# Optimization experiments

Hardware: AMD Instinct MI355X
Metric: run time of the kernel (lower is better)

The kernel has to match this reference:

```python
import jax, jax.numpy as jnp
import numpy as np

N_NODES = 100000
N_EDGES = 1600000
IN_DIM = 128
OUT_DIM = 128
LEAKY_SLOPE = 0.01  # torch nn.LeakyReLU default


def setup_inputs() -> dict:
    key = jax.random.key(0)
    k1, k2, k3, k4 = jax.random.split(key, 4)
    x = jax.random.normal(k1, (N_NODES, IN_DIM), dtype=jnp.float32)
    edge_index = jax.random.randint(k2, (2, N_EDGES), 0, N_NODES, dtype=jnp.int64)
    edge_attr = jax.random.uniform(k3, (N_EDGES,), dtype=jnp.float32)
    # Linear params (xavier_uniform weight, zero bias)
    limit = np.sqrt(6.0 / (IN_DIM + OUT_DIM)).astype(np.float32)
    W = jax.random.uniform(k4, (OUT_DIM, IN_DIM), minval=-limit, maxval=limit, dtype=jnp.float32)
    b = jnp.zeros((OUT_DIM,), dtype=jnp.float32)
    return {"x": x, "edge_index": edge_index, "edge_attr": edge_attr, "W": W, "b": b}


def reference(x, edge_index, edge_attr, W, b):
    src = edge_index[0]  # x_j (source nodes)
    dst = edge_index[1]  # aggregation index (target nodes)
    # message: gather source features, scale by per-edge scalar  [E, D]
    msg = x[src] * edge_attr[:, None]
    # aggregate: scatter-add over target index  [N, D]
    agg = jax.ops.segment_sum(msg, dst, num_segments=N_NODES)
    # update: Linear + LeakyReLU (dropout is identity at p=0 / eval)
    out = agg @ W.T + b
    return jnp.where(out >= 0, out, LEAKY_SLOPE * out)
```

## Files before the change

### kernel.cpp

```cpp
#include <hip/hip_runtime.h>

#define N_NODES 100000
#define N_EDGES 1600000
#define DIM 128
#define LEAKY 0.01f
#define RS_STRIDE 132
#define WS_STRIDE 132
#define NBUCKET 391
#define SB_EDGES 4096
#define NSB 391

typedef short bf16x8 __attribute__((ext_vector_type(8)));
typedef float f32x4 __attribute__((ext_vector_type(4)));

static __device__ __forceinline__ unsigned short f2bf(float f) {
  unsigned int u = __float_as_uint(f);
  u = (u + 0x7fffu + ((u >> 16) & 1u)) >> 16;
  return (unsigned short)u;
}

__global__ __launch_bounds__(512) void sort_local_kernel(
    const int* __restrict__ ei, const float* __restrict__ attr,
    int2* __restrict__ binned, unsigned short* __restrict__ counts,
    int* __restrict__ srcOff) {
  __shared__ int hist[NBUCKET];
  __shared__ int cursor[NBUCKET];
  __shared__ int scanBuf[512];
  __shared__ int2 stage[SB_EDGES];

  const int t = threadIdx.x;
  const int blk = blockIdx.x;
  const int base = blk * SB_EDGES;
  const int n = min(SB_EDGES, N_EDGES - base);

  if (t < NBUCKET) hist[t] = 0;
  __syncthreads();

  int myP[8];
  int myB[8];
  float myA[8];
#pragma unroll
  for (int k = 0; k < 8; ++k) {
    int i = t + k * 512;
    if (i < n) {
      int e = base + i;
      int s = ei[e];
      int d = ei[N_EDGES + e];
      myA[k] = attr[e];
      myB[k] = d >> 8;
      myP[k] = s | ((d & 255) << 17);
      atomicAdd(&hist[myB[k]], 1);
    } else {
      myB[k] = -1;
    }
  }
  __syncthreads();

  int v = (t < NBUCKET) ? hist[t] : 0;
  scanBuf[t] = v;
  __syncthreads();
  for (int off = 1; off < 512; off <<= 1) {
    int u = (t >= off) ? scanBuf[t - off] : 0;
    __syncthreads();
    scanBuf[t] += u;
    __syncthreads();
  }
  if (t < NBUCKET) {
    int excl = scanBuf[t] - v;
    cursor[t] = excl;
    counts[(size_t)t * NSB + blk] = (unsigned short)v;
    srcOff[(size_t)t * NSB + blk] = base + excl;
  }
  __syncthreads();

#pragma unroll
  for (int k = 0; k < 8; ++k) {
    if (myB[k] >= 0) {
      int loc = atomicAdd(&cursor[myB[k]], 1);
      stage[loc] = make_int2(myP[k], __float_as_int(myA[k]));
    }
  }
  __syncthreads();

  for (int i = t; i < n; i += 512) binned[base + i] = stage[i];
}

__global__ __launch_bounds__(128) void bucket_count_kernel(
    const unsigned short* __restrict__ counts, int* __restrict__ bucketCount,
    const float* __restrict__ W, bf16x8* __restrict__ wfrag,
    const float4* __restrict__ x4, ushort4* __restrict__ xb4) {
  __shared__ int red[128];
  const int b = blockIdx.x;
  const int t = threadIdx.x;

  if (b < NBUCKET) {
    int s = 0;
    for (int sb = t; sb < NSB; sb += 128) s += counts[(size_t)b * NSB + sb];
    red[t] = s;
    __syncthreads();
    for (int off = 64; off > 0; off >>= 1) {
      if (t < off) red[t] += red[t + off];
      __syncthreads();
    }
    if (t == 0) bucketCount[b] = red[0];
  } else {
    const int gid = (b - NBUCKET) * 128 + t;
    const int lane = gid & 63;
    const int q = (gid >> 6) & 3;
    const int nt = gid >> 8;
    const int n = nt * 16 + (lane & 15);
    const int kb = q * 32 + ((lane >> 4) & 3) * 8;
    const float4 f0 = *(const float4*)(W + n * DIM + kb);
    const float4 f1 = *(const float4*)(W + n * DIM + kb + 4);
    bf16x8 frag;
    frag[0] = (short)f2bf(f0.x); frag[1] = (short)f2bf(f0.y);
    frag[2] = (short)f2bf(f0.z); frag[3] = (short)f2bf(f0.w);
    frag[4] = (short)f2bf(f1.x); frag[5] = (short)f2bf(f1.y);
    frag[6] = (short)f2bf(f1.z); frag[7] = (short)f2bf(f1.w);
    wfrag[gid] = frag;
  }

  if (xb4) {
    const int stride = (NBUCKET + 16) * 128;
    for (int i = b * 128 + t; i < (N_NODES * DIM) / 4; i += stride) {
      float4 vv = x4[i];
      ushort4 o;
      o.x = f2bf(vv.x); o.y = f2bf(vv.y); o.z = f2bf(vv.z); o.w = f2bf(vv.w);
      xb4[i] = o;
    }
  }
}

__global__ __launch_bounds__(512) void bucket_scan_kernel(
    const int* __restrict__ bucketCount, int* __restrict__ bucketBase) {
  __shared__ int s[512];
  const int t = threadIdx.x;
  int v = (t < NBUCKET) ? bucketCount[t] : 0;
  s[t] = v;
  __syncthreads();
  for (int off = 1; off < 512; off <<= 1) {
    int u = (t >= off) ? s[t - off] : 0;
    __syncthreads();
    s[t] += u;
    __syncthreads();
  }
  if (t < NBUCKET) bucketBase[t] = s[t] - v;
}

__global__ __launch_bounds__(448) void passB_kernel(
    const int2* __restrict__ binned, const unsigned short* __restrict__ counts,
    const int* __restrict__ srcOff, const int* __restrict__ bucketBase,
    int2* __restrict__ csr, int* __restrict__ row_ptr) {
  __shared__ int runSrc[NSB];
  __shared__ int runLen[NSB];
  __shared__ int hist[256];
  __shared__ int cur[256];
  __shared__ int scanBuf[256];

  const int b = blockIdx.x;
  const int t = threadIdx.x;

  if (t < NSB) {
    runSrc[t] = srcOff[(size_t)b * NSB + t];
    runLen[t] = (int)counts[(size_t)b * NSB + t];
  }
  if (t < 256) hist[t] = 0;
  __syncthreads();

  if (t < NSB) {
    const int src = runSrc[t];
    const int len = runLen[t];
    for (int j = 0; j < len; ++j) {
      int px = binned[src + j].x;
      atomicAdd(&hist[(px >> 17) & 255], 1);
    }
  }
  __syncthreads();

  int hv = (t < 256) ? hist[t] : 0;
  if (t < 256) scanBuf[t] = hv;
  __syncthreads();
  for (int off = 1; off < 256; off <<= 1) {
    int u = 0;
    if (t < 256 && t >= off) u = scanBuf[t - off];
    __syncthreads();
    if (t < 256) scanBuf[t] += u;
    __syncthreads();
  }
  const int bb = bucketBase[b];
  if (t < 256) {
    int excl = scanBuf[t] - hv;
    cur[t] = excl;
    int node = b * 256 + t;
    if (node < N_NODES) row_ptr[node] = bb + excl;
  }
  if (b == 0 && t == 0) row_ptr[N_NODES] = N_EDGES;
  __syncthreads();

  if (t < NSB) {
    const int src = runSrc[t];
    const int len = runLen[t];
    for (int j = 0; j < len; ++j) {
      int2 rec = binned[src + j];
      int ld = (rec.x >> 17) & 255;
      int pos = bb + atomicAdd(&cur[ld], 1);
      csr[pos] = make_int2(rec.x & 0x1FFFF, rec.y);
    }
  }
}

__global__ __launch_bounds__(256) void gather_aggb_kernel(
    const unsigned short* __restrict__ xb, const int* __restrict__ row_ptr,
    const int2* __restrict__ csr, unsigned int* __restrict__ aggB) {
  const int w = threadIdx.x >> 6;
  const int lane = threadIdx.x & 63;
  const int nA = blockIdx.x * 8 + w * 2;
  const int nB = nA + 1;

  int a = row_ptr[nA];
  const int aEnd = row_ptr[nA + 1];
  int b = row_ptr[nB];
  const int bEnd = row_ptr[nB + 1];

  float2 accA = make_float2(0.f, 0.f);
  float2 accB = make_float2(0.f, 0.f);

  while (a + 5 < aEnd && b + 5 < bEnd) {
    int2 ea[6], eb[6];
#pragma unroll
    for (int k = 0; k < 6; ++k) {
      ea[k] = csr[a + k];
      eb[k] = csr[b + k];
    }
    unsigned int ua[6], ub[6];
#pragma unroll
    for (int k = 0; k < 6; ++k) {
      ua[k] = *(const unsigned int*)(xb + (size_t)ea[k].x * DIM + lane * 2);
      ub[k] = *(const unsigned int*)(xb + (size_t)eb[k].x * DIM + lane * 2);
    }
#pragma unroll
    for (int k = 0; k < 6; ++k) {
      float fa = __int_as_float(ea[k].y);
      float fb = __int_as_float(eb[k].y);
      accA.x += __uint_as_float(ua[k] << 16) * fa;
      accA.y += __uint_as_float(ua[k] & 0xffff0000u) * fa;
      accB.x += __uint_as_float(ub[k] << 16) * fb;
      accB.y += __uint_as_float(ub[k] & 0xffff0000u) * fb;
    }
    a += 6;
    b += 6;
  }

  for (; a + 3 < aEnd; a += 4) {
    int2 e[4];
#pragma unroll
    for (int k = 0; k < 4; ++k) e[k] = csr[a + k];
    unsigned int u[4];
#pragma unroll
    for (int k = 0; k < 4; ++k)
      u[k] = *(const unsigned int*)(xb + (size_t)e[k].x * DIM + lane * 2);
#pragma unroll
    for (int k = 0; k < 4; ++k) {
      float f = __int_as_float(e[k].y);
      accA.x += __uint_as_float(u[k] << 16) * f;
      accA.y += __uint_as_float(u[k] & 0xffff0000u) * f;
    }
  }
  for (; a < aEnd; ++a) {
    int2 e0 = csr[a];
    float f0 = __int_as_float(e0.y);
    unsigned int u0 = *(const unsigned int*)(xb + (size_t)e0.x * DIM + lane * 2);
    accA.x += __uint_as_float(u0 << 16) * f0;
    accA.y += __uint_as_float(u0 & 0xffff0000u) * f0;
  }

  for (; b + 3 < bEnd; b += 4) {
    int2 e[4];
#pragma unroll
    for (int k = 0; k < 4; ++k) e[k] = csr[b + k];
    unsigned int u[4];
#pragma unroll
    for (int k = 0; k < 4; ++k)
      u[k] = *(const unsigned int*)(xb + (size_t)e[k].x * DIM + lane * 2);
#pragma unroll
    for (int k = 0; k < 4; ++k) {
      float f = __int_as_float(e[k].y);
      accB.x += __uint_as_float(u[k] << 16) * f;
      accB.y += __uint_as_float(u[k] & 0xffff0000u) * f;
    }
  }
  for (; b < bEnd; ++b) {
    int2 e0 = csr[b];
    float f0 = __int_as_float(e0.y);
    unsigned int u0 = *(const unsigned int*)(xb + (size_t)e0.x * DIM + lane * 2);
    accB.x += __uint_as_float(u0 << 16) * f0;
    accB.y += __uint_as_float(u0 & 0xffff0000u) * f0;
  }

  aggB[(size_t)nA * 64 + lane] =
      (unsigned int)f2bf(accA.x) | ((unsigned int)f2bf(accA.y) << 16);
  aggB[(size_t)nB * 64 + lane] =
      (unsigned int)f2bf(accB.x) | ((unsigned int)f2bf(accB.y) << 16);
}

__global__ __launch_bounds__(256) void gather_bf16_kernel(
    const unsigned short* __restrict__ xb, const int* __restrict__ row_ptr,
    const int2* __restrict__ csr, float* __restrict__ out) {
  const int node = blockIdx.x * 4 + (threadIdx.x >> 6);
  const int lane = threadIdx.x & 63;

  const int beg = row_ptr[node];
  const int end = row_ptr[node + 1];

  float2 acc = make_float2(0.f, 0.f);
  int e = beg;
  for (; e + 3 < end; e += 4) {
    int2 e0 = csr[e];
    int2 e1 = csr[e + 1];
    int2 e2 = csr[e + 2];
    int2 e3 = csr[e + 3];
    unsigned int u0 = *(const unsigned int*)(xb + (size_t)e0.x * DIM + lane * 2);
    unsigned int u1 = *(const unsigned int*)(xb + (size_t)e1.x * DIM + lane * 2);
    unsigned int u2 = *(const unsigned int*)(xb + (size_t)e2.x * DIM + lane * 2);
    unsigned int u3 = *(const unsigned int*)(xb + (size_t)e3.x * DIM + lane * 2);
    float a0 = __int_as_float(e0.y), a1 = __int_as_float(e1.y);
    float a2 = __int_as_float(e2.y), a3 = __int_as_float(e3.y);
    acc.x += __uint_as_float(u0 << 16) * a0;
    acc.y += __uint_as_float(u0 & 0xffff0000u) * a0;
    acc.x += __uint_as_float(u1 << 16) * a1;
    acc.y += __uint_as_float(u1 & 0xffff0000u) * a1;
    acc.x += __uint_as_float(u2 << 16) * a2;
    acc.y += __uint_as_float(u2 & 0xffff0000u) * a2;
    acc.x += __uint_as_float(u3 << 16) * a3;
    acc.y += __uint_as_float(u3 & 0xffff0000u) * a3;
  }
  for (; e < end; ++e) {
    int2 e0 = csr[e];
    float a0 = __int_as_float(e0.y);
    unsigned int u0 = *(const unsigned int*)(xb + (size_t)e0.x * DIM + lane * 2);
    acc.x += __uint_as_float(u0 << 16) * a0;
    acc.y += __uint_as_float(u0 & 0xffff0000u) * a0;
  }
  *(float2*)(out + (size_t)node * DIM + lane * 2) = acc;
}

__global__ __launch_bounds__(256) void gather_f32_kernel(
    const float* __restrict__ x, const int* __restrict__ row_ptr,
    const int2* __restrict__ csr, float* __restrict__ out) {
  const int node = blockIdx.x * 4 + (threadIdx.x >> 6);
  const int lane = threadIdx.x & 63;

  const int beg = row_ptr[node];
  const int end = row_ptr[node + 1];

  float2 acc = make_float2(0.f, 0.f);
  int e = beg;
  for (; e + 3 < end; e += 4) {
    int2 e0 = csr[e];
    int2 e1 = csr[e + 1];
    int2 e2 = csr[e + 2];
    int2 e3 = csr[e + 3];
    float2 v0 = *(const float2*)(x + (size_t)e0.x * DIM + lane * 2);
    float2 v1 = *(const float2*)(x + (size_t)e1.x * DIM + lane * 2);
    float2 v2 = *(const float2*)(x + (size_t)e2.x * DIM + lane * 2);
    float2 v3 = *(const float2*)(x + (size_t)e3.x * DIM + lane * 2);
    float a0 = __int_as_float(e0.y), a1 = __int_as_float(e1.y);
    float a2 = __int_as_float(e2.y), a3 = __int_as_float(e3.y);
    acc.x += v0.x * a0; acc.y += v0.y * a0;
    acc.x += v1.x * a1; acc.y += v1.y * a1;
    acc.x += v2.x * a2; acc.y += v2.y * a2;
    acc.x += v3.x * a3; acc.y += v3.y * a3;
  }
  for (; e < end; ++e) {
    int2 e0 = csr[e];
    float a0 = __int_as_float(e0.y);
    float2 v0 = *(const float2*)(x + (size_t)e0.x * DIM + lane * 2);
    acc.x += v0.x * a0; acc.y += v0.y * a0;
  }
  *(float2*)(out + (size_t)node * DIM + lane * 2) = acc;
}

__global__ __launch_bounds__(256) void linear_mfma_bf16_kernel(
    const unsigned short* __restrict__ aggB, const bf16x8* __restrict__ wfrag,
    const float* __restrict__ bias, float* __restrict__ out) {
  const int wave = threadIdx.x >> 6;
  const int lane = threadIdx.x & 63;
  const int r0 = (blockIdx.x * 4 + wave) * 16;
  if (r0 >= N_NODES) return;

  const int m = lane & 15;
  const int quad = lane >> 4;
  const int row = r0 + m;

  bf16x8 afrag[4];
#pragma unroll
  for (int q = 0; q < 4; ++q) {
    afrag[q] = *(const bf16x8*)(aggB + (size_t)row * DIM + q * 32 + quad * 8);
  }

#pragma unroll
  for (int nt = 0; nt < 8; ++nt) {
    const float bv = bias[nt * 16 + m];
    f32x4 acc = {bv, bv, bv, bv};
#pragma unroll
    for (int q = 0; q < 4; ++q) {
      bf16x8 bfrag = wfrag[(nt * 4 + q) * 64 + lane];
      acc = __builtin_amdgcn_mfma_f32_16x16x32_bf16(afrag[q], bfrag, acc, 0, 0, 0);
    }
    const int col = nt * 16 + m;
#pragma unroll
    for (int i = 0; i < 4; ++i) {
      float v = acc[i];
      v = v >= 0.f ? v : v * LEAKY;
      out[(size_t)(r0 + quad * 4 + i) * DIM + col] = v;
    }
  }
}

__global__ __launch_bounds__(256) void linear_mfma_kernel(
    const float* __restrict__ agg, const bf16x8* __restrict__ wfrag,
    const float* __restrict__ bias, float* __restrict__ out) {
  const int wave = threadIdx.x >> 6;
  const int lane = threadIdx.x & 63;
  const int r0 = (blockIdx.x * 4 + wave) * 16;
  if (r0 >= N_NODES) return;

  const int m = lane & 15;
  const int quad = lane >> 4;
  const int row = r0 + m;

  bf16x8 afrag[4];
#pragma unroll
  for (int q = 0; q < 4; ++q) {
    const float* ap = agg + (size_t)row * DIM + q * 32 + quad * 8;
    const float4 f0 = *(const float4*)(ap);
    const float4 f1 = *(const float4*)(ap + 4);
    afrag[q][0] = (short)f2bf(f0.x); afrag[q][1] = (short)f2bf(f0.y);
    afrag[q][2] = (short)f2bf(f0.z); afrag[q][3] = (short)f2bf(f0.w);
    afrag[q][4] = (short)f2bf(f1.x); afrag[q][5] = (short)f2bf(f1.y);
    afrag[q][6] = (short)f2bf(f1.z); afrag[q][7] = (short)f2bf(f1.w);
  }

#pragma unroll
  for (int nt = 0; nt < 8; ++nt) {
    const float bv = bias[nt * 16 + m];
    f32x4 acc = {bv, bv, bv, bv};
#pragma unroll
    for (int q = 0; q < 4; ++q) {
      bf16x8 bfrag = wfrag[(nt * 4 + q) * 64 + lane];
      acc = __builtin_amdgcn_mfma_f32_16x16x32_bf16(afrag[q], bfrag, acc, 0, 0, 0);
    }
    const int col = nt * 16 + m;
#pragma unroll
    for (int i = 0; i < 4; ++i) {
      float v = acc[i];
      v = v >= 0.f ? v : v * LEAKY;
      out[(size_t)(r0 + quad * 4 + i) * DIM + col] = v;
    }
  }
}

__global__ __launch_bounds__(256) void scatter_kernel(
    const float* __restrict__ x, const int* __restrict__ ei,
    const float* __restrict__ attr, float* __restrict__ agg) {
  int gid = blockIdx.x * blockDim.x + threadIdx.x;
  int e = gid >> 5;
  int f = (gid & 31) * 4;
  if (e >= N_EDGES) return;
  int s = ei[e];
  int d = ei[N_EDGES + e];
  float a = attr[e];
  const float4 xv = *(const float4*)(x + (size_t)s * DIM + f);
  float* dp = agg + (size_t)d * DIM + f;
  atomicAdd(dp + 0, xv.x * a);
  atomicAdd(dp + 1, xv.y * a);
  atomicAdd(dp + 2, xv.z * a);
  atomicAdd(dp + 3, xv.w * a);
}

__global__ __launch_bounds__(256, 2) void linear_kernel(
    const float* __restrict__ agg, const float* __restrict__ W,
    const float* __restrict__ bias, float* __restrict__ out) {
  __shared__ float Rs[32 * RS_STRIDE];
  __shared__ float Ws[64 * WS_STRIDE];

  const int tid = threadIdx.x;
  const int c = (tid & 31) * 4;
  const int rg = tid >> 5;
  const size_t rowBase = (size_t)blockIdx.x * 32;

  {
    const int lr = tid >> 3;
    const int col = (tid & 7) * 16;
    const float4* src = (const float4*)(agg + (rowBase + lr) * DIM + col);
#pragma unroll
    for (int j = 0; j < 4; ++j) {
      *(float4*)(Rs + lr * RS_STRIDE + col + j * 4) = src[j];
    }
  }

  const float4 bv = *(const float4*)(bias + c);
  float4 acc0 = bv, acc1 = bv, acc2 = bv, acc3 = bv;

  for (int half = 0; half < 2; ++half) {
    __syncthreads();
    {
      const int k0 = tid >> 7;
      const int o = tid & 127;
#pragma unroll
      for (int kk = k0; kk < 64; kk += 2) {
        Ws[kk * WS_STRIDE + o] = W[o * DIM + half * 64 + kk];
      }
    }
    __syncthreads();

    const float* rs0 = Rs + (rg * 4 + 0) * RS_STRIDE + half * 64;
    const float* rs1 = Rs + (rg * 4 + 1) * RS_STRIDE + half * 64;
    const float* rs2 = Rs + (rg * 4 + 2) * RS_STRIDE + half * 64;
    const float* rs3 = Rs + (rg * 4 + 3) * RS_STRIDE + half * 64;

#pragma unroll 8
    for (int k4 = 0; k4 < 16; ++k4) {
      const float4 v0 = *(const float4*)(rs0 + k4 * 4);
      const float4 v1 = *(const float4*)(rs1 + k4 * 4);
      const float4 v2 = *(const float4*)(rs2 + k4 * 4);
      const float4 v3 = *(const float4*)(rs3 + k4 * 4);
      const float4 w0 = *(const float4*)(Ws + (k4 * 4 + 0) * WS_STRIDE + c);
      const float4 w1 = *(const float4*)(Ws + (k4 * 4 + 1) * WS_STRIDE + c);
      const float4 w2 = *(const float4*)(Ws + (k4 * 4 + 2) * WS_STRIDE + c);
      const float4 w3 = *(const float4*)(Ws + (k4 * 4 + 3) * WS_STRIDE + c);

#define FMA4(acc, v)                                               \
      acc.x += v.x * w0.x + v.y * w1.x + v.z * w2.x + v.w * w3.x;  \
      acc.y += v.x * w0.y + v.y * w1.y + v.z * w2.y + v.w * w3.y;  \
      acc.z += v.x * w0.z + v.y * w1.z + v.z * w2.z + v.w * w3.z;  \
      acc.w += v.x * w0.w + v.y * w1.w + v.z * w2.w + v.w * w3.w;
      FMA4(acc0, v0)
      FMA4(acc1, v1)
      FMA4(acc2, v2)
      FMA4(acc3, v3)
#undef FMA4
    }
  }

#define LEAKY4(acc)                                   \
  acc.x = acc.x >= 0.f ? acc.x : acc.x * LEAKY;       \
  acc.y = acc.y >= 0.f ? acc.y : acc.y * LEAKY;       \
  acc.z = acc.z >= 0.f ? acc.z : acc.z * LEAKY;       \
  acc.w = acc.w >= 0.f ? acc.w : acc.w * LEAKY;
  LEAKY4(acc0) LEAKY4(acc1) LEAKY4(acc2) LEAKY4(acc3)
#undef LEAKY4

  const int row0 = (int)rowBase + rg * 4;
  *(float4*)(out + (size_t)(row0 + 0) * DIM + c) = acc0;
  *(float4*)(out + (size_t)(row0 + 1) * DIM + c) = acc1;
  *(float4*)(out + (size_t)(row0 + 2) * DIM + c) = acc2;
  *(float4*)(out + (size_t)(row0 + 3) * DIM + c) = acc3;
}

extern "C" void kernel_launch(void* const* d_in, const int* in_sizes, int n_in,
                              void* d_out, int out_size, void* d_ws, size_t ws_size,
                              hipStream_t stream) {
  const float* x = (const float*)d_in[0];
  const int* ei = (const int*)d_in[1];
  const float* attr = (const float*)d_in[2];
  const float* W = (const float*)d_in[3];
  const float* b = (const float*)d_in[4];
  float* out = (float*)d_out;

  const size_t offBinned = 0;
  const size_t offCounts = 12812288;
  const size_t offSrcOff = offCounts + 305920;
  const size_t offBCount = offSrcOff + 611584;
  const size_t offBBase  = offBCount + 1792;
  const size_t offCsr    = offBBase + 1792;
  const size_t offRowPtr = offCsr + 12812288;
  const size_t offWfrag  = offRowPtr + 400128;
  const size_t sortNeed  = offWfrag + 32768;
  const size_t offXb     = sortNeed;
  const size_t fullNeed  = offXb + 25600000;
  const size_t offAggB   = fullNeed;
  const size_t bf16Need  = offAggB + 25600000;

  if (ws_size >= sortNeed) {
    char* ws = (char*)d_ws;
    int2* binned = (int2*)(ws + offBinned);
    unsigned short* counts = (unsigned short*)(ws + offCounts);
    int* srcOff = (int*)(ws + offSrcOff);
    int* bucketCount = (int*)(ws + offBCount);
    int* bucketBase = (int*)(ws + offBBase);
    int2* csr = (int2*)(ws + offCsr);
    int* row_ptr = (int*)(ws + offRowPtr);
    bf16x8* wfrag = (bf16x8*)(ws + offWfrag);
    const bool haveXb = ws_size >= fullNeed;
    const bool haveAggB = ws_size >= bf16Need;
    unsigned short* xb = haveXb ? (unsigned short*)(ws + offXb) : nullptr;
    unsigned int* aggB = haveAggB ? (unsigned int*)(ws + offAggB) : nullptr;

    sort_local_kernel<<<NSB, 512, 0, stream>>>(ei, attr, binned, counts, srcOff);
    bucket_count_kernel<<<NBUCKET + 16, 128, 0, stream>>>(
        counts, bucketCount, W, wfrag, (const float4*)x, (ushort4*)xb);
    bucket_scan_kernel<<<1, 512, 0, stream>>>(bucketCount, bucketBase);
    passB_kernel<<<NBUCKET, 448, 0, stream>>>(binned, counts, srcOff, bucketBase,
                                              csr, row_ptr);
    if (haveAggB) {
      gather_aggb_kernel<<<N_NODES / 8, 256, 0, stream>>>(xb, row_ptr, csr, aggB);
      linear_mfma_bf16_kernel<<<(N_NODES + 63) / 64, 256, 0, stream>>>(
          (const unsigned short*)aggB, wfrag, b, out);
    } else if (haveXb) {
      gather_bf16_kernel<<<N_NODES / 4, 256, 0, stream>>>(xb, row_ptr, csr, out);
      linear_mfma_kernel<<<(N_NODES + 63) / 64, 256, 0, stream>>>(out, wfrag, b, out);
    } else {
      gather_f32_kernel<<<N_NODES / 4, 256, 0, stream>>>(x, row_ptr, csr, out);
      linear_mfma_kernel<<<(N_NODES + 63) / 64, 256, 0, stream>>>(out, wfrag, b, out);
    }
  } else {
    hipMemsetAsync(out, 0, (size_t)N_NODES * DIM * sizeof(float), stream);
    scatter_kernel<<<(N_EDGES * 32) / 256, 256, 0, stream>>>(x, ei, attr, out);
    linear_kernel<<<N_NODES / 32, 256, 0, stream>>>(out, W, b, out);
  }
}
```

Before: 246.8 us.

## Replace two-pass bucket sort CSR build with global atomic counting sort

Replaces the local-sort-plus-bucket-merge CSR construction with a direct counting sort. It builds a global degree histogram with atomics, scans it into row pointers, and places each edge through an atomicAdd on a per-node cursor. The x-to-bf16 and W-fragment conversions become separate kernels, and the fallback gather/linear variants are removed. This drops the intermediate binned array and the serial per-run loops in passB. In exchange it relies on heavy global atomics and scattered writes, and edge order within a row becomes nondeterministic.

```diff
diff --git a/kernel.cpp b/kernel.cpp
--- a/kernel.cpp
+++ b/kernel.cpp
@@ -7,8 +7,6 @@
 #define RS_STRIDE 132
 #define WS_STRIDE 132
 #define NBUCKET 391
-#define SB_EDGES 4096
-#define NSB 391
 
 typedef short bf16x8 __attribute__((ext_vector_type(8)));
 typedef float f32x4 __attribute__((ext_vector_type(4)));
@@ -19,116 +17,31 @@
   return (unsigned short)u;
 }
 
-__global__ __launch_bounds__(512) void sort_local_kernel(
-    const int* __restrict__ ei, const float* __restrict__ attr,
-    int2* __restrict__ binned, unsigned short* __restrict__ counts,
-    int* __restrict__ srcOff) {
-  __shared__ int hist[NBUCKET];
-  __shared__ int cursor[NBUCKET];
-  __shared__ int scanBuf[512];
-  __shared__ int2 stage[SB_EDGES];
-
-  const int t = threadIdx.x;
-  const int blk = blockIdx.x;
-  const int base = blk * SB_EDGES;
-  const int n = min(SB_EDGES, N_EDGES - base);
-
-  if (t < NBUCKET) hist[t] = 0;
-  __syncthreads();
-
-  int myP[8];
-  int myB[8];
-  float myA[8];
-#pragma unroll
-  for (int k = 0; k < 8; ++k) {
-    int i = t + k * 512;
-    if (i < n) {
-      int e = base + i;
-      int s = ei[e];
-      int d = ei[N_EDGES + e];
-      myA[k] = attr[e];
-      myB[k] = d >> 8;
-      myP[k] = s | ((d & 255) << 17);
-      atomicAdd(&hist[myB[k]], 1);
-    } else {
-      myB[k] = -1;
-    }
-  }
-  __syncthreads();
-
-  int v = (t < NBUCKET) ? hist[t] : 0;
-  scanBuf[t] = v;
-  __syncthreads();
-  for (int off = 1; off < 512; off <<= 1) {
-    int u = (t >= off) ? scanBuf[t - off] : 0;
-    __syncthreads();
-    scanBuf[t] += u;
-    __syncthreads();
-  }
-  if (t < NBUCKET) {
-    int excl = scanBuf[t] - v;
-    cursor[t] = excl;
-    counts[(size_t)t * NSB + blk] = (unsigned short)v;
-    srcOff[(size_t)t * NSB + blk] = base + excl;
-  }
-  __syncthreads();
-
-#pragma unroll
-  for (int k = 0; k < 8; ++k) {
-    if (myB[k] >= 0) {
-      int loc = atomicAdd(&cursor[myB[k]], 1);
-      stage[loc] = make_int2(myP[k], __float_as_int(myA[k]));
-    }
-  }
-  __syncthreads();
-
-  for (int i = t; i < n; i += 512) binned[base + i] = stage[i];
-}
-
-__global__ __launch_bounds__(128) void bucket_count_kernel(
-    const unsigned short* __restrict__ counts, int* __restrict__ bucketCount,
-    const float* __restrict__ W, bf16x8* __restrict__ wfrag,
-    const float4* __restrict__ x4, ushort4* __restrict__ xb4) {
-  __shared__ int red[128];
+__global__ __launch_bounds__(256) void deg_hist_kernel(
+    const int* __restrict__ ei, int* __restrict__ deg) {
+  const int e = blockIdx.x * 256 + threadIdx.x;
+  const int d = ei[N_EDGES + e];
+  atomicAdd(&deg[d], 1);
+}
+
+__global__ __launch_bounds__(256) void scanA_kernel(
+    const int* __restrict__ deg, int* __restrict__ row_ptr,
+    int* __restrict__ bucketCount) {
+  __shared__ int s[256];
   const int b = blockIdx.x;
   const int t = threadIdx.x;
-
-  if (b < NBUCKET) {
-    int s = 0;
-    for (int sb = t; sb < NSB; sb += 128) s += counts[(size_t)b * NSB + sb];
-    red[t] = s;
-    __syncthreads();
-    for (int off = 64; off > 0; off >>= 1) {
-      if (t < off) red[t] += red[t + off];
-      __syncthreads();
-    }
-    if (t == 0) bucketCount[b] = red[0];
-  } else {
-    const int gid = (b - NBUCKET) * 128 + t;
-    const int lane = gid & 63;
-    const int q = (gid >> 6) & 3;
-    const int nt = gid >> 8;
-    const int n = nt * 16 + (lane & 15);
-    const int kb = q * 32 + ((lane >> 4) & 3) * 8;
-    const float4 f0 = *(const float4*)(W + n * DIM + kb);
-    const float4 f1 = *(const float4*)(W + n * DIM + kb + 4);
-    bf16x8 frag;
-    frag[0] = (short)f2bf(f0.x); frag[1] = (short)f2bf(f0.y);
-    frag[2] = (short)f2bf(f0.z); frag[3] = (short)f2bf(f0.w);
-    frag[4] = (short)f2bf(f1.x); frag[5] = (short)f2bf(f1.y);
-    frag[6] = (short)f2bf(f1.z); frag[7] = (short)f2bf(f1.w);
-    wfrag[gid] = frag;
-  }
-
-  if (xb4) {
-    const int stride = (NBUCKET + 16) * 128;
-    for (int i = b * 128 + t; i < (N_NODES * DIM) / 4; i += stride) {
-      float4 vv = x4[i];
-      ushort4 o;
-      o.x = f2bf(vv.x); o.y = f2bf(vv.y); o.z = f2bf(vv.z); o.w = f2bf(vv.w);
-      xb4[i] = o;
-    }
-  }
+  const int node = b * 256 + t;
+  const int v = (node < N_NODES) ? deg[node] : 0;
+  s[t] = v;
+  __syncthreads();
+  for (int off = 1; off < 256; off <<= 1) {
+    int u = (t >= off) ? s[t - off] : 0;
+    __syncthreads();
+    s[t] += u;
+    __syncthreads();
+  }
+  if (node < N_NODES) row_ptr[node] = s[t] - v;
+  if (t == 0) bucketCount[b] = s[255];
 }
 
 __global__ __launch_bounds__(512) void bucket_scan_kernel(
@@ -147,66 +60,56 @@
   if (t < NBUCKET) bucketBase[t] = s[t] - v;
 }
 
-__global__ __launch_bounds__(448) void passB_kernel(
-    const int2* __restrict__ binned, const unsigned short* __restrict__ counts,
-    const int* __restrict__ srcOff, const int* __restrict__ bucketBase,
-    int2* __restrict__ csr, int* __restrict__ row_ptr) {
-  __shared__ int runSrc[NSB];
-  __shared__ int runLen[NSB];
-  __shared__ int hist[256];
-  __shared__ int cur[256];
-  __shared__ int scanBuf[256];
-
+__global__ __launch_bounds__(256) void scanB_kernel(
+    int* __restrict__ row_ptr, const int* __restrict__ bucketBase,
+    int* __restrict__ cur) {
   const int b = blockIdx.x;
   const int t = threadIdx.x;
-
-  if (t < NSB) {
-    runSrc[t] = srcOff[(size_t)b * NSB + t];
-    runLen[t] = (int)counts[(size_t)b * NSB + t];
-  }
-  if (t < 256) hist[t] = 0;
-  __syncthreads();
-
-  if (t < NSB) {
-    const int src = runSrc[t];
-    const int len = runLen[t];
-    for (int j = 0; j < len; ++j) {
-      int px = binned[src + j].x;
-      atomicAdd(&hist[(px >> 17) & 255], 1);
-    }
-  }
-  __syncthreads();
-
-  int hv = (t < 256) ? hist[t] : 0;
-  if (t < 256) scanBuf[t] = hv;
-  __syncthreads();
-  for (int off = 1; off < 256; off <<= 1) {
-    int u = 0;
-    if (t < 256 && t >= off) u = scanBuf[t - off];
-    __syncthreads();
-    if (t < 256) scanBuf[t] += u;
-    __syncthreads();
-  }
-  const int bb = bucketBase[b];
-  if (t < 256) {
-    int excl = scanBuf[t] - hv;
-    cur[t] = excl;
-    int node = b * 256 + t;
-    if (node < N_NODES) row_ptr[node] = bb + excl;
+  const int node = b * 256 + t;
+  if (node < N_NODES) {
+    const int rp = row_ptr[node] + bucketBase[b];
+    row_ptr[node] = rp;
+    cur[node] = rp;
   }
   if (b == 0 && t == 0) row_ptr[N_NODES] = N_EDGES;
-  __syncthreads();
-
-  if (t < NSB) {
-    const int src = runSrc[t];
-    const int len = runLen[t];
-    for (int j = 0; j < len; ++j) {
-      int2 rec = binned[src + j];
-      int ld = (rec.x >> 17) & 255;
-      int pos = bb + atomicAdd(&cur[ld], 1);
-      csr[pos] = make_int2(rec.x & 0x1FFFF, rec.y);
-    }
-  }
+}
+
+__global__ __launch_bounds__(256) void place_edges_kernel(
+    const int* __restrict__ ei, const float* __restrict__ attr,
+    int* __restrict__ cur, int2* __restrict__ csr) {
+  const int e = blockIdx.x * 256 + threadIdx.x;
+  const int s = ei[e];
+  const int d = ei[N_EDGES + e];
+  const float a = attr[e];
+  const int pos = atomicAdd(&cur[d], 1);
+  csr[pos] = make_int2(s, __float_as_int(a));
+}
+
+__global__ __launch_bounds__(256) void x2b_kernel(
+    const float4* __restrict__ x, ushort4* __restrict__ xb) {
+  const int i = blockIdx.x * 256 + threadIdx.x;
+  float4 v = x[i];
+  ushort4 o;
+  o.x = f2bf(v.x); o.y = f2bf(v.y); o.z = f2bf(v.z); o.w = f2bf(v.w);
+  xb[i] = o;
+}
+
+__global__ __launch_bounds__(256) void w_frag_kernel(
+    const float* __restrict__ W, bf16x8* __restrict__ wfrag) {
+  const int gid = blockIdx.x * 256 + threadIdx.x;
+  const int lane = gid & 63;
+  const int q = (gid >> 6) & 3;
+  const int nt = gid >> 8;
+  const int n = nt * 16 + (lane & 15);
+  const int kb = q * 32 + ((lane >> 4) & 3) * 8;
+  const float4 f0 = *(const float4*)(W + n * DIM + kb);
+  const float4 f1 = *(const float4*)(W + n * DIM + kb + 4);
+  bf16x8 frag;
+  frag[0] = (short)f2bf(f0.x); frag[1] = (short)f2bf(f0.y);
+  frag[2] = (short)f2bf(f0.z); frag[3] = (short)f2bf(f0.w);
+  frag[4] = (short)f2bf(f1.x); frag[5] = (short)f2bf(f1.y);
+  frag[6] = (short)f2bf(f1.z); frag[7] = (short)f2bf(f1.w);
+  wfrag[gid] = frag;
 }
 
 __global__ __launch_bounds__(256) void gather_aggb_kernel(
@@ -303,83 +206,6 @@
       (unsigned int)f2bf(accB.x) | ((unsigned int)f2bf(accB.y) << 16);
 }
 
-__global__ __launch_bounds__(256) void gather_bf16_kernel(
-    const unsigned short* __restrict__ xb, const int* __restrict__ row_ptr,
-    const int2* __restrict__ csr, float* __restrict__ out) {
-  const int node = blockIdx.x * 4 + (threadIdx.x >> 6);
-  const int lane = threadIdx.x & 63;
-
-  const int beg = row_ptr[node];
-  const int end = row_ptr[node + 1];
-
-  float2 acc = make_float2(0.f, 0.f);
-  int e = beg;
-  for (; e + 3 < end; e += 4) {
-    int2 e0 = csr[e];
-    int2 e1 = csr[e + 1];
-    int2 e2 = csr[e + 2];
-    int2 e3 = csr[e + 3];
-    unsigned int u0 = *(const unsigned int*)(xb + (size_t)e0.x * DIM + lane * 2);
-    unsigned int u1 = *(const unsigned int*)(xb + (size_t)e1.x * DIM + lane * 2);
-    unsigned int u2 = *(const unsigned int*)(xb + (size_t)e2.x * DIM + lane * 2);
-    unsigned int u3 = *(const unsigned int*)(xb + (size_t)e3.x * DIM + lane * 2);
-    float a0 = __int_as_float(e0.y), a1 = __int_as_float(e1.y);
-    float a2 = __int_as_float(e2.y), a3 = __int_as_float(e3.y);
-    acc.x += __uint_as_float(u0 << 16) * a0;
-    acc.y += __uint_as_float(u0 & 0xffff0000u) * a0;
-    acc.x += __uint_as_float(u1 << 16) * a1;
-    acc.y += __uint_as_float(u1 & 0xffff0000u) * a1;
-    acc.x += __uint_as_float(u2 << 16) * a2;
-    acc.y += __uint_as_float(u2 & 0xffff0000u) * a2;
-    acc.x += __uint_as_float(u3 << 16) * a3;
-    acc.y += __uint_as_float(u3 & 0xffff0000u) * a3;
-  }
-  for (; e < end; ++e) {
-    int2 e0 = csr[e];
-    float a0 = __int_as_float(e0.y);
-    unsigned int u0 = *(const unsigned int*)(xb + (size_t)e0.x * DIM + lane * 2);
-    acc.x += __uint_as_float(u0 << 16) * a0;
-    acc.y += __uint_as_float(u0 & 0xffff0000u) * a0;
-  }
-  *(float2*)(out + (size_t)node * DIM + lane * 2) = acc;
-}
-
-__global__ __launch_bounds__(256) void gather_f32_kernel(
-    const float* __restrict__ x, const int* __restrict__ row_ptr,
-    const int2* __restrict__ csr, float* __restrict__ out) {
-  const int node = blockIdx.x * 4 + (threadIdx.x >> 6);
-  const int lane = threadIdx.x & 63;
-
-  const int beg = row_ptr[node];
-  const int end = row_ptr[node + 1];
-
-  float2 acc = make_float2(0.f, 0.f);
-  int e = beg;
-  for (; e + 3 < end; e += 4) {
-    int2 e0 = csr[e];
-    int2 e1 = csr[e + 1];
-    int2 e2 = csr[e + 2];
-    int2 e3 = csr[e + 3];
-    float2 v0 = *(const float2*)(x + (size_t)e0.x * DIM + lane * 2);
-    float2 v1 = *(const float2*)(x + (size_t)e1.x * DIM + lane * 2);
-    float2 v2 = *(const float2*)(x + (size_t)e2.x * DIM + lane * 2);
-    float2 v3 = *(const float2*)(x + (size_t)e3.x * DIM + lane * 2);
-    float a0 = __int_as_float(e0.y), a1 = __int_as_float(e1.y);
-    float a2 = __int_as_float(e2.y), a3 = __int_as_float(e3.y);
-    acc.x += v0.x * a0; acc.y += v0.y * a0;
-    acc.x += v1.x * a1; acc.y += v1.y * a1;
-    acc.x += v2.x * a2; acc.y += v2.y * a2;
-    acc.x += v3.x * a3; acc.y += v3.y * a3;
-  }
-  for (; e < end; ++e) {
-    int2 e0 = csr[e];
-    float a0 = __int_as_float(e0.y);
-    float2 v0 = *(const float2*)(x + (size_t)e0.x * DIM + lane * 2);
-    acc.x += v0.x * a0; acc.y += v0.y * a0;
-  }
-  *(float2*)(out + (size_t)node * DIM + lane * 2) = acc;
-}
-
 __global__ __launch_bounds__(256) void linear_mfma_bf16_kernel(
     const unsigned short* __restrict__ aggB, const bf16x8* __restrict__ wfrag,
     const float* __restrict__ bias, float* __restrict__ out) {
@@ -396,49 +222,6 @@
 #pragma unroll
   for (int q = 0; q < 4; ++q) {
     afrag[q] = *(const bf16x8*)(aggB + (size_t)row * DIM + q * 32 + quad * 8);
-  }
-
-#pragma unroll
-  for (int nt = 0; nt < 8; ++nt) {
-    const float bv = bias[nt * 16 + m];
-    f32x4 acc = {bv, bv, bv, bv};
-#pragma unroll
-    for (int q = 0; q < 4; ++q) {
-      bf16x8 bfrag = wfrag[(nt * 4 + q) * 64 + lane];
-      acc = __builtin_amdgcn_mfma_f32_16x16x32_bf16(afrag[q], bfrag, acc, 0, 0, 0);
-    }
-    const int col = nt * 16 + m;
-#pragma unroll
-    for (int i = 0; i < 4; ++i) {
-      float v = acc[i];
-      v = v >= 0.f ? v : v * LEAKY;
-      out[(size_t)(r0 + quad * 4 + i) * DIM + col] = v;
-    }
-  }
-}
-
-__global__ __launch_bounds__(256) void linear_mfma_kernel(
-    const float* __restrict__ agg, const bf16x8* __restrict__ wfrag,
-    const float* __restrict__ bias, float* __restrict__ out) {
-  const int wave = threadIdx.x >> 6;
-  const int lane = threadIdx.x & 63;
-  const int r0 = (blockIdx.x * 4 + wave) * 16;
-  if (r0 >= N_NODES) return;
-
-  const int m = lane & 15;
-  const int quad = lane >> 4;
-  const int row = r0 + m;
-
-  bf16x8 afrag[4];
-#pragma unroll
-  for (int q = 0; q < 4; ++q) {
-    const float* ap = agg + (size_t)row * DIM + q * 32 + quad * 8;
-    const float4 f0 = *(const float4*)(ap);
-    const float4 f1 = *(const float4*)(ap + 4);
-    afrag[q][0] = (short)f2bf(f0.x); afrag[q][1] = (short)f2bf(f0.y);
-    afrag[q][2] = (short)f2bf(f0.z); afrag[q][3] = (short)f2bf(f0.w);
-    afrag[q][4] = (short)f2bf(f1.x); afrag[q][5] = (short)f2bf(f1.y);
-    afrag[q][6] = (short)f2bf(f1.z); afrag[q][7] = (short)f2bf(f1.w);
   }
 
 #pragma unroll
@@ -568,52 +351,40 @@
   const float* b = (const float*)d_in[4];
   float* out = (float*)d_out;
 
-  const size_t offBinned = 0;
-  const size_t offCounts = 12812288;
-  const size_t offSrcOff = offCounts + 305920;
-  const size_t offBCount = offSrcOff + 611584;
+  const size_t offCsr    = 0;
+  const size_t offRowPtr = 12800000;
+  const size_t offDeg    = offRowPtr + 400128;
+  const size_t offCur    = offDeg + 400128;
+  const size_t offBCount = offCur + 400128;
   const size_t offBBase  = offBCount + 1792;
-  const size_t offCsr    = offBBase + 1792;
-  const size_t offRowPtr = offCsr + 12812288;
-  const size_t offWfrag  = offRowPtr + 400128;
-  const size_t sortNeed  = offWfrag + 32768;
-  const size_t offXb     = sortNeed;
-  const size_t fullNeed  = offXb + 25600000;
-  const size_t offAggB   = fullNeed;
-  const size_t bf16Need  = offAggB + 25600000;
-
-  if (ws_size >= sortNeed) {
+  const size_t offWfrag  = offBBase + 1792;
+  const size_t offXb     = offWfrag + 32768;
+  const size_t offAggB   = offXb + 25600000;
+  const size_t fullNeed  = offAggB + 25600000;
+
+  if (ws_size >= fullNeed) {
     char* ws = (char*)d_ws;
-    int2* binned = (int2*)(ws + offBinned);
-    unsigned short* counts = (unsigned short*)(ws + offCounts);
-    int* srcOff = (int*)(ws + offSrcOff);
+    int2* csr = (int2*)(ws + offCsr);
+    int* row_ptr = (int*)(ws + offRowPtr);
+    int* deg = (int*)(ws + offDeg);
+    int* cur = (int*)(ws + offCur);
     int* bucketCount = (int*)(ws + offBCount);
     int* bucketBase = (int*)(ws + offBBase);
-    int2* csr = (int2*)(ws + offCsr);
-    int* row_ptr = (int*)(ws + offRowPtr);
     bf16x8* wfrag = (bf16x8*)(ws + offWfrag);
-    const bool haveXb = ws_size >= fullNeed;
-    const bool haveAggB = ws_size >= bf16Need;
-    unsigned short* xb = haveXb ? (unsigned short*)(ws + offXb) : nullptr;
-    unsigned int* aggB = haveAggB ? (unsigned int*)(ws + offAggB) : nullptr;
-
-    sort_local_kernel<<<NSB, 512, 0, stream>>>(ei, attr, binned, counts, srcOff);
-    bucket_count_kernel<<<NBUCKET + 16, 128, 0, stream>>>(
-        counts, bucketCount, W, wfrag, (const float4*)x, (ushort4*)xb);
+    unsigned short* xb = (unsigned short*)(ws + offXb);
+    unsigned int* aggB = (unsigned int*)(ws + offAggB);
+
+    hipMemsetAsync(deg, 0, (size_t)N_NODES * sizeof(int), stream);
+    deg_hist_kernel<<<N_EDGES / 256, 256, 0, stream>>>(ei, deg);
+    scanA_kernel<<<NBUCKET, 256, 0, stream>>>(deg, row_ptr, bucketCount);
     bucket_scan_kernel<<<1, 512, 0, stream>>>(bucketCount, bucketBase);
-    passB_kernel<<<NBUCKET, 448, 0, stream>>>(binned, counts, srcOff, bucketBase,
-                                              csr, row_ptr);
-    if (haveAggB) {
-      gather_aggb_kernel<<<N_NODES / 8, 256, 0, stream>>>(xb, row_ptr, csr, aggB);
-      linear_mfma_bf16_kernel<<<(N_NODES + 63) / 64, 256, 0, stream>>>(
-          (const unsigned short*)aggB, wfrag, b, out);
-    } else if (haveXb) {
-      gather_bf16_kernel<<<N_NODES / 4, 256, 0, stream>>>(xb, row_ptr, csr, out);
-      linear_mfma_kernel<<<(N_NODES + 63) / 64, 256, 0, stream>>>(out, wfrag, b, out);
-    } else {
-      gather_f32_kernel<<<N_NODES / 4, 256, 0, stream>>>(x, row_ptr, csr, out);
-      linear_mfma_kernel<<<(N_NODES + 63) / 64, 256, 0, stream>>>(out, wfrag, b, out);
-    }
+    scanB_kernel<<<NBUCKET, 256, 0, stream>>>(row_ptr, bucketBase, cur);
+    place_edges_kernel<<<N_EDGES / 256, 256, 0, stream>>>(ei, attr, cur, csr);
+    x2b_kernel<<<12500, 256, 0, stream>>>((const float4*)x, (ushort4*)xb);
+    w_frag_kernel<<<8, 256, 0, stream>>>(W, wfrag);
+    gather_aggb_kernel<<<N_NODES / 8, 256, 0, stream>>>(xb, row_ptr, csr, aggB);
+    linear_mfma_bf16_kernel<<<(N_NODES + 63) / 64, 256, 0, stream>>>(
+        (const unsigned short*)aggB, wfrag, b, out);
   } else {
     hipMemsetAsync(out, 0, (size_t)N_NODES * DIM * sizeof(float), stream);
     scatter_kernel<<<(N_EDGES * 32) / 256, 256, 0, stream>>>(x, ei, attr, out);
```

Result: slower. 379.2 us (+53.7%).

## Fuse bucket count, scan, and CSR build into one kernel with conversions

Applied to the files above, without the earlier changes.

Removes the separate bucket_count and bucket_scan kernels. Each CSR-build block now computes its own bucket base by summing all preceding counts directly. The W-fragment and x-to-bf16 conversions run as extra blocks in the same launch, which cuts two kernel launches and their serialization gaps. In exchange, each bucket block does a redundant prefix sum over up to ~150K counts, with total work growing quadratically across blocks, and the conversion blocks compete with the build blocks for the GPU.

```diff
diff --git a/kernel.cpp b/kernel.cpp
--- a/kernel.cpp
+++ b/kernel.cpp
@@ -9,6 +9,7 @@
 #define NBUCKET 391
 #define SB_EDGES 4096
 #define NSB 391
+#define X2B_CHUNKS 7143
 
 typedef short bf16x8 __attribute__((ext_vector_type(8)));
 typedef float f32x4 __attribute__((ext_vector_type(4)));
@@ -85,87 +86,76 @@
   for (int i = t; i < n; i += 512) binned[base + i] = stage[i];
 }
 
-__global__ __launch_bounds__(128) void bucket_count_kernel(
-    const unsigned short* __restrict__ counts, int* __restrict__ bucketCount,
-    const float* __restrict__ W, bf16x8* __restrict__ wfrag,
-    const float4* __restrict__ x4, ushort4* __restrict__ xb4) {
-  __shared__ int red[128];
-  const int b = blockIdx.x;
+__global__ __launch_bounds__(448) void build_convert_kernel(
+    const int2* __restrict__ binned, const unsigned short* __restrict__ counts,
+    const int* __restrict__ srcOff, int2* __restrict__ csr,
+    int* __restrict__ row_ptr, const float* __restrict__ W,
+    bf16x8* __restrict__ wfrag, const float4* __restrict__ x4,
+    ushort4* __restrict__ xb4) {
+  const int blk = blockIdx.x;
   const int t = threadIdx.x;
 
-  if (b < NBUCKET) {
-    int s = 0;
-    for (int sb = t; sb < NSB; sb += 128) s += counts[(size_t)b * NSB + sb];
-    red[t] = s;
-    __syncthreads();
-    for (int off = 64; off > 0; off >>= 1) {
-      if (t < off) red[t] += red[t + off];
-      __syncthreads();
-    }
-    if (t == 0) bucketCount[b] = red[0];
-  } else {
-    const int gid = (b - NBUCKET) * 128 + t;
-    const int lane = gid & 63;
-    const int q = (gid >> 6) & 3;
-    const int nt = gid >> 8;
-    const int n = nt * 16 + (lane & 15);
-    const int kb = q * 32 + ((lane >> 4) & 3) * 8;
-    const float4 f0 = *(const float4*)(W + n * DIM + kb);
-    const float4 f1 = *(const float4*)(W + n * DIM + kb + 4);
-    bf16x8 frag;
-    frag[0] = (short)f2bf(f0.x); frag[1] = (short)f2bf(f0.y);
-    frag[2] = (short)f2bf(f0.z); frag[3] = (short)f2bf(f0.w);
-    frag[4] = (short)f2bf(f1.x); frag[5] = (short)f2bf(f1.y);
-    frag[6] = (short)f2bf(f1.z); frag[7] = (short)f2bf(f1.w);
-    wfrag[gid] = frag;
-  }
-
-  if (xb4) {
-    const int stride = (NBUCKET + 16) * 128;
-    for (int i = b * 128 + t; i < (N_NODES * DIM) / 4; i += stride) {
-      float4 vv = x4[i];
-      ushort4 o;
-      o.x = f2bf(vv.x); o.y = f2bf(vv.y); o.z = f2bf(vv.z); o.w = f2bf(vv.w);
-      xb4[i] = o;
-    }
-  }
-}
-
-__global__ __launch_bounds__(512) void bucket_scan_kernel(
-    const int* __restrict__ bucketCount, int* __restrict__ bucketBase) {
-  __shared__ int s[512];
-  const int t = threadIdx.x;
-  int v = (t < NBUCKET) ? bucketCount[t] : 0;
-  s[t] = v;
-  __syncthreads();
-  for (int off = 1; off < 512; off <<= 1) {
-    int u = (t >= off) ? s[t - off] : 0;
-    __syncthreads();
-    s[t] += u;
-    __syncthreads();
-  }
-  if (t < NBUCKET) bucketBase[t] = s[t] - v;
-}
-
-__global__ __launch_bounds__(448) void passB_kernel(
-    const int2* __restrict__ binned, const unsigned short* __restrict__ counts,
-    const int* __restrict__ srcOff, const int* __restrict__ bucketBase,
-    int2* __restrict__ csr, int* __restrict__ row_ptr) {
+  if (blk >= NBUCKET) {
+    if (blk < NBUCKET + 8) {
+      if (t < 256) {
+        const int gid = (blk - NBUCKET) * 256 + t;
+        const int lane = gid & 63;
+        const int q = (gid >> 6) & 3;
+        const int nt = gid >> 8;
+        const int n = nt * 16 + (lane & 15);
+        const int kb = q * 32 + ((lane >> 4) & 3) * 8;
+        const float4 f0 = *(const float4*)(W + n * DIM + kb);
+        const float4 f1 = *(const float4*)(W + n * DIM + kb + 4);
+        bf16x8 frag;
+        frag[0] = (short)f2bf(f0.x); frag[1] = (short)f2bf(f0.y);
+        frag[2] = (short)f2bf(f0.z); frag[3] = (short)f2bf(f0.w);
+        frag[4] = (short)f2bf(f1.x); frag[5] = (short)f2bf(f1.y);
+        frag[6] = (short)f2bf(f1.z); frag[7] = (short)f2bf(f1.w);
+        wfrag[gid] = frag;
+      }
+    } else {
+      const int i = (blk - NBUCKET - 8) * 448 + t;
+      if (i < (N_NODES * DIM) / 4) {
+        float4 vv = x4[i];
+        ushort4 o;
+        o.x = f2bf(vv.x); o.y = f2bf(vv.y); o.z = f2bf(vv.z); o.w = f2bf(vv.w);
+        xb4[i] = o;
+      }
+    }
+    return;
+  }
+
   __shared__ int runSrc[NSB];
   __shared__ int runLen[NSB];
   __shared__ int hist[256];
   __shared__ int cur[256];
   __shared__ int scanBuf[256];
-
-  const int b = blockIdx.x;
-  const int t = threadIdx.x;
+  __shared__ int wsum[7];
+  __shared__ int bbS;
+
+  const int b = blk;
 
   if (t < NSB) {
     runSrc[t] = srcOff[(size_t)b * NSB + t];
     runLen[t] = (int)counts[(size_t)b * NSB + t];
   }
   if (t < 256) hist[t] = 0;
-  __syncthreads();
+
+  {
+    int part = 0;
+    const int limit = b * NSB;
+    for (int i = t; i < limit; i += 448) part += (int)counts[i];
+#pragma unroll
+    for (int off = 32; off > 0; off >>= 1) part += __shfl_down(part, off);
+    if ((t & 63) == 0) wsum[t >> 6] = part;
+  }
+  __syncthreads();
+  if (t == 0) {
+    int s = 0;
+#pragma unroll
+    for (int w = 0; w < 7; ++w) s += wsum[w];
+    bbS = s;
+  }
 
   if (t < NSB) {
     const int src = runSrc[t];
@@ -187,7 +177,7 @@
     if (t < 256) scanBuf[t] += u;
     __syncthreads();
   }
-  const int bb = bucketBase[b];
+  const int bb = bbS;
   if (t < 256) {
     int excl = scanBuf[t] - hv;
     cur[t] = excl;
@@ -571,9 +561,7 @@
   const size_t offBinned = 0;
   const size_t offCounts = 12812288;
   const size_t offSrcOff = offCounts + 305920;
-  const size_t offBCount = offSrcOff + 611584;
-  const size_t offBBase  = offBCount + 1792;
-  const size_t offCsr    = offBBase + 1792;
+  const size_t offCsr    = offSrcOff + 611584;
   const size_t offRowPtr = offCsr + 12812288;
   const size_t offWfrag  = offRowPtr + 400128;
   const size_t sortNeed  = offWfrag + 32768;
@@ -587,8 +575,6 @@
     int2* binned = (int2*)(ws + offBinned);
     unsigned short* counts = (unsigned short*)(ws + offCounts);
     int* srcOff = (int*)(ws + offSrcOff);
-    int* bucketCount = (int*)(ws + offBCount);
-    int* bucketBase = (int*)(ws + offBBase);
     int2* csr = (int2*)(ws + offCsr);
     int* row_ptr = (int*)(ws + offRowPtr);
     bf16x8* wfrag = (bf16x8*)(ws + offWfrag);
@@ -598,11 +584,10 @@
     unsigned int* aggB = haveAggB ? (unsigned int*)(ws + offAggB) : nullptr;
 
     sort_local_kernel<<<NSB, 512, 0, stream>>>(ei, attr, binned, counts, srcOff);
-    bucket_count_kernel<<<NBUCKET + 16, 128, 0, stream>>>(
-        counts, bucketCount, W, wfrag, (const float4*)x, (ushort4*)xb);
-    bucket_scan_kernel<<<1, 512, 0, stream>>>(bucketCount, bucketBase);
-    passB_kernel<<<NBUCKET, 448, 0, stream>>>(binned, counts, srcOff, bucketBase,
-                                              csr, row_ptr);
+    const int buildGrid = haveXb ? (NBUCKET + 8 + X2B_CHUNKS) : (NBUCKET + 8);
+    build_convert_kernel<<<buildGrid, 448, 0, stream>>>(
+        binned, counts, srcOff, csr, row_ptr, W, wfrag,
+        (const float4*)x, (ushort4*)xb);
     if (haveAggB) {
       gather_aggb_kernel<<<N_NODES / 8, 256, 0, stream>>>(xb, row_ptr, csr, aggB);
       linear_mfma_bf16_kernel<<<(N_NODES + 63) / 64, 256, 0, stream>>>(
```

Result: no change. 250.7 us (+1.6%).
